# Kernel optimization log

Measured on AMD Instinct MI355X. Metric: run time of the kernel, lower is better.

## Reference

```python
import jax, jax.numpy as jnp
import numpy as np

N_STATE = 64
SEQ_L = 4096
BATCH, HCH = 16, 512
DT_MIN, DT_MAX = 0.001, 0.1


def _make_DPLR_HiPPO(N):
    # HiPPO-LegS matrix and its NPLR -> DPLR decomposition (annotated-s4).
    P = np.sqrt(1 + 2 * np.arange(N))
    A = P[:, None] * P[None, :]
    A = np.tril(A) - np.diag(np.arange(N))
    nhippo = -A
    p = 0.5 * np.sqrt(2 * np.arange(1, N + 1) + 1.0)
    q = 2 * p
    S = nhippo + p[:, None] * q[None, :]
    Lambda, V = np.linalg.eig(S)
    Vc = V.conj().T
    p_t = Vc @ p
    q_t = Vc @ q.conj()
    return Lambda, p_t, q_t, Vc


def _ri(z):
    return np.stack([z.real, z.imag], axis=-1).astype(np.float32)


def setup_inputs() -> dict:
    key = jax.random.key(0)
    k_u, k_ct, k_b, k_d, k_ls = jax.random.split(key, 5)
    Lambda, p, q, Vc = _make_DPLR_HiPPO(N_STATE)
    u = jax.random.normal(k_u, (BATCH, HCH, SEQ_L), dtype=jnp.float32)
    # lecun_normal params (fan_in = N)
    Ct_ri = jax.random.normal(k_ct, (1, N_STATE, 2), dtype=jnp.float32) / np.sqrt(N_STATE)
    Bp = jax.random.normal(k_b, (N_STATE, 1), dtype=jnp.float32) / np.sqrt(N_STATE)
    D = jax.random.uniform(k_d, (1,), dtype=jnp.float32)
    log_step = jax.random.uniform(
        k_ls, (1,), dtype=jnp.float32,
        minval=np.log(DT_MIN), maxval=np.log(DT_MAX))
    return {
        "u": u,
        "Lambda_ri": jnp.asarray(_ri(Lambda)),
        "p_ri": jnp.asarray(_ri(p)),
        "q_ri": jnp.asarray(_ri(q)),
        "Vc_ri": jnp.asarray(_ri(Vc)),
        "Ct_ri": Ct_ri,
        "Bp": Bp,
        "D": D,
        "log_step": log_step,
    }


def _cplx(x_ri):
    return x_ri[..., 0] + 1j * x_ri[..., 1]


def _s4_kernel(Lambda, p, q, B, Ct, step, L):
    # DPLR generating function evaluated at the L roots of unity (K_gen_DPLR
    # + conv_from_gen), vectorized over frequencies.
    Omega = jnp.exp((-2j * jnp.pi) * (jnp.arange(L) / L))          # (L,)
    g = (2.0 / step) * ((1.0 - Omega) / (1.0 + Omega))             # (L,)
    c = 2.0 / (1.0 + Omega)                                        # (L,)
    denom = g[:, None] - Lambda[None, :]                           # (L, N)
    cauchy = lambda v: (v[None, :] / denom).sum(-1)                # (L,)
    k00 = cauchy(Ct.conj() * B)
    k01 = cauchy(Ct.conj() * p)
    k10 = cauchy(q.conj() * B)
    k11 = cauchy(q.conj() * p)
    at_roots = c * (k00 - k01 * (1.0 / (1.0 + k11)) * k10)
    return jnp.fft.ifft(at_roots, L).real                          # (L,)


def reference(u, Lambda_ri, p_ri, q_ri, Vc_ri, Ct_ri, Bp, D, log_step):
    L = u.shape[-1]
    Lambda = _cplx(Lambda_ri)
    p = _cplx(p_ri)
    q = _cplx(q_ri)
    Vc = _cplx(Vc_ri)
    Ct = _cplx(Ct_ri).reshape(-1)                  # (N,)
    B = (Vc @ Bp.astype(Vc.dtype)).reshape(-1)     # (N,) complex
    step = jnp.exp(log_step)[0]
    K = _s4_kernel(Lambda, p, q, B, Ct, step, L).astype(u.dtype)   # (L,)
    # non-circular convolution via zero-padded FFT along the last axis
    n = 2 * L
    y = jnp.fft.irfft(jnp.fft.rfft(u, n=n) * jnp.fft.rfft(K, n=n), n=n)[..., :L]
    return y + D[0] * u
```

## Files before the change

### kernel.cpp

```cpp
#include <hip/hip_runtime.h>
#include <math.h>


#define SEQ_L 4096
#define M4    4096
#define NFFT  8192
#define NST   64
#define NROWS 8192
#define TWO_PI 6.28318530717958647692f

typedef float2 cf;

__device__ __forceinline__ cf cmul(cf a, cf b){ return make_float2(a.x*b.x - a.y*b.y, a.x*b.y + a.y*b.x); }
__device__ __forceinline__ cf cadd(cf a, cf b){ return make_float2(a.x+b.x, a.y+b.y); }
__device__ __forceinline__ cf csub(cf a, cf b){ return make_float2(a.x-b.x, a.y-b.y); }
__device__ __forceinline__ double2 dcmul(double2 a, double2 b) {
  return make_double2(a.x*b.x - a.y*b.y, a.x*b.y + a.y*b.x);
}

__device__ __forceinline__ int s2f(int i){ return i ^ (((i >> 6) & 1) << 3); }
__device__ __forceinline__ int s3f(int i){ return i ^ ((i >> 6) & 7) ^ (((i >> 6) & 1) << 3); }
__device__ __forceinline__ int smf(int i){ return i ^ ((i >> 6) & 7); }
__device__ __forceinline__ int sw(int p){ return p ^ ((p >> 4) & 15); }

template<int S>
__device__ __forceinline__ void r4(cf& a0, cf& a1, cf& a2, cf& a3){
  cf t0 = cadd(a0,a2), t1 = csub(a0,a2);
  cf t2 = cadd(a1,a3), t3 = csub(a1,a3);
  cf w = (S < 0) ? make_float2(t3.y, -t3.x) : make_float2(-t3.y, t3.x);
  a0 = cadd(t0,t2); a2 = csub(t0,t2);
  a1 = cadd(t1,w);  a3 = csub(t1,w);
}

template<int S, bool ZHI, bool LO4=false>
__device__ __forceinline__ void dft8(cf x[8]){
  const float C = 0.70710678118654752f;
  cf e0,e1,e2,e3,o0,o1,o2,o3;
  if (ZHI) {
    cf w  = (S<0)? make_float2(x[2].y,-x[2].x) : make_float2(-x[2].y,x[2].x);
    e0 = cadd(x[0],x[2]); e2 = csub(x[0],x[2]);
    e1 = cadd(x[0],w);    e3 = csub(x[0],w);
    cf w2 = (S<0)? make_float2(x[3].y,-x[3].x) : make_float2(-x[3].y,x[3].x);
    o0 = cadd(x[1],x[3]); o2 = csub(x[1],x[3]);
    o1 = cadd(x[1],w2);   o3 = csub(x[1],w2);
  } else {
    cf a0=x[0],a1=x[2],a2=x[4],a3=x[6];
    r4<S>(a0,a1,a2,a3);  e0=a0;e1=a1;e2=a2;e3=a3;
    cf b0=x[1],b1=x[3],b2=x[5],b3=x[7];
    r4<S>(b0,b1,b2,b3);  o0=b0;o1=b1;o2=b2;o3=b3;
  }
  x[0] = cadd(e0,o0); if (!LO4) x[4] = csub(e0,o0);
  cf t1 = (S<0)? make_float2(C*(o1.x+o1.y), C*(o1.y-o1.x))
               : make_float2(C*(o1.x-o1.y), C*(o1.x+o1.y));
  x[1] = cadd(e1,t1); if (!LO4) x[5] = csub(e1,t1);
  cf t2 = (S<0)? make_float2(o2.y,-o2.x) : make_float2(-o2.y,o2.x);
  x[2] = cadd(e2,t2); if (!LO4) x[6] = csub(e2,t2);
  cf t3 = (S<0)? make_float2(C*(o3.y-o3.x), -C*(o3.x+o3.y))
               : make_float2(-C*(o3.x+o3.y), C*(o3.x-o3.y));
  x[3] = cadd(e3,t3); if (!LO4) x[7] = csub(e3,t3);
}

__device__ __forceinline__ void chain8(cf x[8], float th){
  float sn, cs; __sincosf(th, &sn, &cs);
  cf w1 = make_float2(cs, sn);
  cf w2 = cmul(w1, w1);
  cf w3 = cmul(w2, w1);
  x[1] = cmul(x[1], w1); x[2] = cmul(x[2], w2); x[3] = cmul(x[3], w3);
  cf w4 = cmul(w2, w2);
  cf w5 = cmul(w3, w2);
  cf w6 = cmul(w3, w3);
  cf w7 = cmul(w4, w3);
  x[4] = cmul(x[4], w4); x[5] = cmul(x[5], w5); x[6] = cmul(x[6], w6);
  x[7] = cmul(x[7], w7);
}

__device__ __forceinline__ constexpr float c16t(int d){
  return (d==1)?0.92387953251128675613f:(d==2)?0.70710678118654752440f:
         (d==3)?0.38268343236508977173f:(d==4)?0.f:
         (d==5)?-0.38268343236508977173f:(d==6)?-0.70710678118654752440f:
         -0.92387953251128675613f;
}
__device__ __forceinline__ constexpr float s16t(int d){
  return (d==1)?0.38268343236508977173f:(d==2)?0.70710678118654752440f:
         (d==3)?0.92387953251128675613f:(d==4)?1.f:
         (d==5)?0.92387953251128675613f:(d==6)?0.70710678118654752440f:
         0.38268343236508977173f;
}
template<int S>
__device__ __forceinline__ void tw16(cf x[8], int t000){
  #pragma unroll
  for (int d = 1; d < 8; ++d) {
    float ce = t000 ? c16t(d) : 1.f;
    float se = t000 ? ((S < 0) ? -s16t(d) : s16t(d)) : 0.f;
    cf a = x[d];
    x[d] = make_float2(a.x*ce - a.y*se, a.x*se + a.y*ce);
  }
}

__device__ __forceinline__ void r2_shfl(cf x[8], int tid){
  const float sgn = (tid & 1) ? -1.f : 1.f;
  #pragma unroll
  for (int k = 0; k < 8; ++k) {
    float ox = __shfl_xor(x[k].x, 1, 64);
    float oy = __shfl_xor(x[k].y, 1, 64);
    x[k].x = ox + sgn * x[k].x;
    x[k].y = oy + sgn * x[k].y;
  }
}

__global__ __launch_bounds__(256) void k_at(
    const float* __restrict__ Lam_ri, const float* __restrict__ p_ri,
    const float* __restrict__ q_ri,  const float* __restrict__ Vc_ri,
    const float* __restrict__ Ct_ri, const float* __restrict__ Bp,
    const float* __restrict__ log_step, float2* __restrict__ atroots) {
  __shared__ double2 lam[NST], ctB[NST], ctp[NST], qB[NST], qp[NST];
  __shared__ double stepd;
  int tx = threadIdx.x;
  if (tx < NST) {
    int n = tx;
    double lr = Lam_ri[2*n], li = Lam_ri[2*n+1];
    double pr = p_ri[2*n],  pi = p_ri[2*n+1];
    double qr = q_ri[2*n],  qi = q_ri[2*n+1];
    double cr = Ct_ri[2*n], ci = Ct_ri[2*n+1];
    double br = 0.0, bi = 0.0;
    for (int m = 0; m < NST; ++m) {
      double b = (double)Bp[m];
      br += (double)Vc_ri[2*(n*NST+m)]   * b;
      bi += (double)Vc_ri[2*(n*NST+m)+1] * b;
    }
    lam[n] = make_double2(lr, li);
    ctB[n] = make_double2(cr*br + ci*bi, cr*bi - ci*br);
    ctp[n] = make_double2(cr*pr + ci*pi, cr*pi - ci*pr);
    qB[n]  = make_double2(qr*br + qi*bi, qr*bi - qi*br);
    qp[n]  = make_double2(qr*pr + qi*pi, qr*pi - qi*pr);
  }
  if (tx == 0) stepd = exp((double)log_step[0]);
  __syncthreads();
  int l = blockIdx.x * 256 + tx;
  double ang = -2.0 * M_PI * (double)l / (double)SEQ_L;
  double sn, cs;
  sincos(ang, &sn, &cs);
  double2 onem = make_double2(1.0 - cs, -sn);
  double2 onep = make_double2(1.0 + cs,  sn);
  double den = onep.x*onep.x + onep.y*onep.y;
  double2 ip = make_double2(onep.x/den, -onep.y/den);
  double2 g  = dcmul(onem, ip);
  double tw = 2.0 / stepd;
  g.x *= tw; g.y *= tw;
  double2 cc = make_double2(2.0*ip.x, 2.0*ip.y);
  double2 k00 = make_double2(0,0), k01 = make_double2(0,0);
  double2 k10 = make_double2(0,0), k11 = make_double2(0,0);
  for (int n = 0; n < NST; ++n) {
    double2 L = lam[n];
    double2 d = make_double2(g.x - L.x, g.y - L.y);
    double dd = d.x*d.x + d.y*d.y;
    double2 inv = make_double2(d.x/dd, -d.y/dd);
    double2 v;
    v = ctB[n]; k00.x += v.x*inv.x - v.y*inv.y; k00.y += v.x*inv.y + v.y*inv.x;
    v = ctp[n]; k01.x += v.x*inv.x - v.y*inv.y; k01.y += v.x*inv.y + v.y*inv.x;
    v = qB[n];  k10.x += v.x*inv.x - v.y*inv.y; k10.y += v.x*inv.y + v.y*inv.x;
    v = qp[n];  k11.x += v.x*inv.x - v.y*inv.y; k11.y += v.x*inv.y + v.y*inv.x;
  }
  double2 k11p = make_double2(1.0 + k11.x, k11.y);
  double2 num  = dcmul(k01, k10);
  double dd2 = k11p.x*k11p.x + k11p.y*k11p.y;
  double2 t = make_double2((num.x*k11p.x + num.y*k11p.y)/dd2,
                           (num.y*k11p.x - num.x*k11p.y)/dd2);
  double2 inner = make_double2(k00.x - t.x, k00.y - t.y);
  double2 at = dcmul(cc, inner);
  atroots[l] = make_float2((float)at.x, (float)at.y);
}

__global__ __launch_bounds__(512) void k_kt(const float2* __restrict__ atroots,
                                            float* __restrict__ Kt) {
  int gid  = blockIdx.x * 512 + threadIdx.x;
  int t    = gid >> 6;
  int lane = gid & 63;
  float acc = 0.f;
  for (int l = lane; l < SEQ_L; l += 64) {
    int ph = (l * t) & (SEQ_L - 1);
    float a = (float)ph * (TWO_PI / (float)SEQ_L);
    float sn, cs; __sincosf(a, &sn, &cs);
    float2 v = atroots[l];
    acc += v.x*cs - v.y*sn;
  }
  for (int off = 32; off > 0; off >>= 1) acc += __shfl_down(acc, off, 64);
  if (lane == 0) Kt[t] = acc * (1.0f / (float)SEQ_L);
}

__global__ __launch_bounds__(1024) void k_G(const float* __restrict__ Kt,
                                            float2* __restrict__ G) {
  __shared__ cf lds[NFFT];
  int tid = threadIdx.x;
  cf x[8];
  #pragma unroll
  for (int m = 0; m < 4; ++m) x[m] = make_float2(Kt[tid + 1024*m], 0.f);
  #pragma unroll
  for (int m = 4; m < 8; ++m) x[m] = make_float2(0.f, 0.f);
  const int a1 = tid >> 7, t0 = tid & 127, b2 = (tid >> 4) & 7, t00 = tid & 15;
  const int c3 = (tid >> 1) & 7, t000 = tid & 1;
  dft8<-1, true>(x);
  chain8(x, -TWO_PI * (float)tid / (float)NFFT);
  #pragma unroll
  for (int a = 0; a < 8; ++a) lds[sw(a*1024 + tid)] = x[a];
  __syncthreads();
  #pragma unroll
  for (int r = 0; r < 8; ++r) x[r] = lds[sw(a1*1024 + t0 + 128*r)];
  dft8<-1, false>(x);
  chain8(x, -TWO_PI * (float)t0 / 1024.f);
  __syncthreads();
  #pragma unroll
  for (int b = 0; b < 8; ++b) lds[sw(a1*1024 + b*128 + t0)] = x[b];
  __syncthreads();
  #pragma unroll
  for (int r = 0; r < 8; ++r) x[r] = lds[sw(a1*1024 + b2*128 + t00 + 16*r)];
  dft8<-1, false>(x);
  chain8(x, -TWO_PI * (float)t00 / 128.f);
  __syncthreads();
  #pragma unroll
  for (int c = 0; c < 8; ++c) lds[sw(a1*1024 + b2*128 + c*16 + t00)] = x[c];
  __syncthreads();
  #pragma unroll
  for (int r = 0; r < 8; ++r) x[r] = lds[sw(a1*1024 + b2*128 + c3*16 + t000 + 2*r)];
  dft8<-1, false>(x);
  tw16<-1>(x, t000);
  r2_shfl(x, tid);
  #pragma unroll
  for (int d = 0; d < 8; ++d) {
    int bin = a1 + 8*b2 + 64*c3 + 512*d + 4096*t000;
    if (bin <= M4) G[bin] = x[d];
  }
}

__global__ __launch_bounds__(256) void k_ab(const float2* __restrict__ G,
                                            float4* __restrict__ ab) {
  int idx = blockIdx.x * 256 + threadIdx.x;
  int tidc = idx >> 3, d = idx & 7;
  int k = (tidc >> 6) + 8*((tidc >> 3) & 7) + 64*(tidc & 7) + 512*d;
  double ang = -2.0 * M_PI * (double)k / (double)NFFT;
  double sn, cs; sincos(ang, &sn, &cs);
  double2 a = make_double2(0.5*(1.0 + sn), -0.5*cs);
  double2 b = make_double2(0.5*(1.0 - sn),  0.5*cs);
  double2 p = make_double2(0.5*(1.0 + sn),  0.5*cs);
  double2 q = make_double2(0.5*(1.0 - sn), -0.5*cs);
  float2 gk = G[k];
  float2 gh = G[M4 - k];
  double2 Gk = make_double2(gk.x, gk.y);
  double2 Gh = make_double2(gh.x, -gh.y);
  double2 pa = dcmul(p, a), pb = dcmul(p, b);
  double2 qa = dcmul(q, a), qb = dcmul(q, b);
  double2 al = dcmul(pa, Gk), t1 = dcmul(qb, Gh);
  al.x += t1.x; al.y += t1.y;
  double2 be = dcmul(pb, Gk), t2 = dcmul(qa, Gh);
  be.x += t2.x; be.y += t2.y;
  const double s = 1.0 / (double)M4;
  ab[idx] = make_float4((float)(al.x*s), (float)(al.y*s),
                        (float)(be.x*s), (float)(be.y*s));
}

__global__ __launch_bounds__(512) void k_conv(const float* __restrict__ u,
                                              const float4* __restrict__ ab,
                                              const float* __restrict__ Dp,
                                              float* __restrict__ out) {
  __shared__ cf lds[M4];
  const int tid = threadIdx.x;
  const size_t row = blockIdx.x;
  const float2* ru = (const float2*)(u + row * SEQ_L);
  const int a1 = tid >> 6, t0 = tid & 63, b2 = (tid >> 3) & 7, t00 = tid & 7;

  cf x[8];
  #pragma unroll
  for (int m = 0; m < 4; ++m) { float2 v = ru[tid + 512*m]; x[m] = make_float2(v.x, v.y); }
  #pragma unroll
  for (int m = 4; m < 8; ++m) x[m] = make_float2(0.f, 0.f);

  dft8<-1, true>(x);
  chain8(x, -TWO_PI * (float)tid / (float)M4);
  #pragma unroll
  for (int a = 0; a < 8; ++a) lds[a*512 + tid] = x[a];
  __syncthreads();
  #pragma unroll
  for (int r = 0; r < 8; ++r) x[r] = lds[a1*512 + t0 + 64*r];
  dft8<-1, false>(x);
  chain8(x, -TWO_PI * (float)t0 / 512.f);
  __syncthreads();
  #pragma unroll
  for (int b = 0; b < 8; ++b) lds[s2f(a1*512 + b*64 + t0)] = x[b];
  __syncthreads();
  #pragma unroll
  for (int r = 0; r < 8; ++r) x[r] = lds[s2f(a1*512 + b2*64 + t00 + 8*r)];
  dft8<-1, false>(x);
  chain8(x, -TWO_PI * (float)t00 / 64.f);
  __syncthreads();
  #pragma unroll
  for (int c = 0; c < 8; ++c) lds[s3f(a1*512 + b2*64 + c*8 + t00)] = x[c];
  __syncthreads();
  #pragma unroll
  for (int r = 0; r < 8; ++r) x[r] = lds[s3f(a1*512 + b2*64 + t00*8 + r)];
  dft8<-1, false>(x);
  __syncthreads();

  const int base = a1 + 8*b2 + 64*t00;
  #pragma unroll
  for (int d = 0; d < 8; ++d) lds[smf(base + 512*d)] = x[d];
  __syncthreads();
  const float4* abp = ab + (size_t)tid * 8;
  #pragma unroll
  for (int d = 0; d < 8; ++d) {
    cf t = lds[smf((M4 - base - 512*d) & (M4 - 1))];
    float4 c = abp[d];
    x[d] = make_float2(c.x*x[d].x - c.y*x[d].y + c.z*t.x + c.w*t.y,
                       c.x*x[d].y + c.y*x[d].x + c.w*t.x - c.z*t.y);
  }
  __syncthreads();

  dft8<1, false>(x);
  #pragma unroll
  for (int r = 0; r < 8; ++r) lds[s3f(a1*512 + b2*64 + t00*8 + r)] = x[r];
  __syncthreads();
  #pragma unroll
  for (int c = 0; c < 8; ++c) x[c] = lds[s3f(a1*512 + b2*64 + c*8 + t00)];
  chain8(x, TWO_PI * (float)t00 / 64.f);
  dft8<1, false>(x);
  __syncthreads();
  #pragma unroll
  for (int r = 0; r < 8; ++r) lds[s2f(a1*512 + b2*64 + t00 + 8*r)] = x[r];
  __syncthreads();
  #pragma unroll
  for (int b = 0; b < 8; ++b) x[b] = lds[s2f(a1*512 + b*64 + t0)];
  chain8(x, TWO_PI * (float)t0 / 512.f);
  dft8<1, false>(x);
  __syncthreads();
  #pragma unroll
  for (int r = 0; r < 8; ++r) lds[a1*512 + t0 + 64*r] = x[r];
  __syncthreads();
  #pragma unroll
  for (int a = 0; a < 8; ++a) x[a] = lds[a*512 + tid];
  chain8(x, TWO_PI * (float)tid / (float)M4);
  dft8<1, false, true>(x);

  const float Dv = Dp[0];
  float2* o = (float2*)(out + row * SEQ_L);
  #pragma unroll
  for (int m = 0; m < 4; ++m) {
    float2 uv = ru[tid + 512*m];
    o[tid + 512*m] = make_float2(x[m].x + Dv*uv.x, x[m].y + Dv*uv.y);
  }
}

extern "C" void kernel_launch(void* const* d_in, const int* in_sizes, int n_in,
                              void* d_out, int out_size, void* d_ws, size_t ws_size,
                              hipStream_t stream) {
  const float* u      = (const float*)d_in[0];
  const float* Lam_ri = (const float*)d_in[1];
  const float* p_ri   = (const float*)d_in[2];
  const float* q_ri   = (const float*)d_in[3];
  const float* Vc_ri  = (const float*)d_in[4];
  const float* Ct_ri  = (const float*)d_in[5];
  const float* Bp     = (const float*)d_in[6];
  const float* Dp     = (const float*)d_in[7];
  const float* ls     = (const float*)d_in[8];

  char* ws = (char*)d_ws;
  float2* atroots = (float2*)(ws);
  float*  Kt      = (float*) (ws + 32768);
  float2* G       = (float2*)(ws + 49152);
  float4* ab      = (float4*)(ws + 81936);

  k_at  <<<dim3(SEQ_L/256), dim3(256), 0, stream>>>(Lam_ri, p_ri, q_ri, Vc_ri, Ct_ri, Bp, ls, atroots);
  k_kt  <<<dim3(512),  dim3(512), 0, stream>>>(atroots, Kt);
  k_G   <<<dim3(1),    dim3(1024), 0, stream>>>(Kt, G);
  k_ab  <<<dim3(16),   dim3(256), 0, stream>>>(G, ab);
  k_conv<<<dim3(NROWS), dim3(512), 0, stream>>>(u, ab, Dp, (float*)d_out);
}
```

Measured before the change: 198.6 us.

## Replace direct inverse DFT with in-block FFT and fuse kernel-prep stages

The O(L^2) sincos-based inverse DFT in k_kt is replaced by a radix-8 4096-point inverse FFT inside a single 1024-thread block. That block also performs the 8192-point forward FFT and the real-FFT split coefficients (former k_G and k_ab), passing intermediates through LDS instead of global memory. This removes two kernel launches and the quadratic DFT work. The cost is that the inverse FFT runs on only one workgroup, with half its threads idle during that phase, so the serial prep latency on one CU grows.

New measurement: 184.3 us (median of 2 runs). 7.2% less time.

```diff
diff --git a/kernel.cpp b/kernel.cpp
--- a/kernel.cpp
+++ b/kernel.cpp
@@ -171,91 +171,126 @@
   atroots[l] = make_float2((float)at.x, (float)at.y);
 }
 
-__global__ __launch_bounds__(512) void k_kt(const float2* __restrict__ atroots,
-                                            float* __restrict__ Kt) {
-  int gid  = blockIdx.x * 512 + threadIdx.x;
-  int t    = gid >> 6;
-  int lane = gid & 63;
-  float acc = 0.f;
-  for (int l = lane; l < SEQ_L; l += 64) {
-    int ph = (l * t) & (SEQ_L - 1);
-    float a = (float)ph * (TWO_PI / (float)SEQ_L);
-    float sn, cs; __sincosf(a, &sn, &cs);
-    float2 v = atroots[l];
-    acc += v.x*cs - v.y*sn;
-  }
-  for (int off = 32; off > 0; off >>= 1) acc += __shfl_down(acc, off, 64);
-  if (lane == 0) Kt[t] = acc * (1.0f / (float)SEQ_L);
-}
-
-__global__ __launch_bounds__(1024) void k_G(const float* __restrict__ Kt,
-                                            float2* __restrict__ G) {
-  __shared__ cf lds[NFFT];
-  int tid = threadIdx.x;
+__global__ __launch_bounds__(1024) void k_Gab(const float2* __restrict__ at,
+                                              float4* __restrict__ ab) {
+  __shared__ cf lds8[NFFT];
+  float* ktf = (float*)(lds8 + 4096);
+  const int tid = threadIdx.x;
+  const bool act = tid < 512;
+  const int a14 = tid >> 6, t04 = tid & 63, b24 = (tid >> 3) & 7, t004 = tid & 7;
   cf x[8];
-  #pragma unroll
-  for (int m = 0; m < 4; ++m) x[m] = make_float2(Kt[tid + 1024*m], 0.f);
-  #pragma unroll
-  for (int m = 4; m < 8; ++m) x[m] = make_float2(0.f, 0.f);
-  const int a1 = tid >> 7, t0 = tid & 127, b2 = (tid >> 4) & 7, t00 = tid & 15;
-  const int c3 = (tid >> 1) & 7, t000 = tid & 1;
-  dft8<-1, true>(x);
-  chain8(x, -TWO_PI * (float)tid / (float)NFFT);
-  #pragma unroll
-  for (int a = 0; a < 8; ++a) lds[sw(a*1024 + tid)] = x[a];
-  __syncthreads();
-  #pragma unroll
-  for (int r = 0; r < 8; ++r) x[r] = lds[sw(a1*1024 + t0 + 128*r)];
-  dft8<-1, false>(x);
-  chain8(x, -TWO_PI * (float)t0 / 1024.f);
-  __syncthreads();
-  #pragma unroll
-  for (int b = 0; b < 8; ++b) lds[sw(a1*1024 + b*128 + t0)] = x[b];
-  __syncthreads();
-  #pragma unroll
-  for (int r = 0; r < 8; ++r) x[r] = lds[sw(a1*1024 + b2*128 + t00 + 16*r)];
-  dft8<-1, false>(x);
-  chain8(x, -TWO_PI * (float)t00 / 128.f);
-  __syncthreads();
-  #pragma unroll
-  for (int c = 0; c < 8; ++c) lds[sw(a1*1024 + b2*128 + c*16 + t00)] = x[c];
-  __syncthreads();
-  #pragma unroll
-  for (int r = 0; r < 8; ++r) x[r] = lds[sw(a1*1024 + b2*128 + c3*16 + t000 + 2*r)];
-  dft8<-1, false>(x);
-  tw16<-1>(x, t000);
-  r2_shfl(x, tid);
-  #pragma unroll
-  for (int d = 0; d < 8; ++d) {
-    int bin = a1 + 8*b2 + 64*c3 + 512*d + 4096*t000;
-    if (bin <= M4) G[bin] = x[d];
-  }
-}
-
-__global__ __launch_bounds__(256) void k_ab(const float2* __restrict__ G,
-                                            float4* __restrict__ ab) {
-  int idx = blockIdx.x * 256 + threadIdx.x;
-  int tidc = idx >> 3, d = idx & 7;
-  int k = (tidc >> 6) + 8*((tidc >> 3) & 7) + 64*(tidc & 7) + 512*d;
-  double ang = -2.0 * M_PI * (double)k / (double)NFFT;
-  double sn, cs; sincos(ang, &sn, &cs);
-  double2 a = make_double2(0.5*(1.0 + sn), -0.5*cs);
-  double2 b = make_double2(0.5*(1.0 - sn),  0.5*cs);
-  double2 p = make_double2(0.5*(1.0 + sn),  0.5*cs);
-  double2 q = make_double2(0.5*(1.0 - sn), -0.5*cs);
-  float2 gk = G[k];
-  float2 gh = G[M4 - k];
-  double2 Gk = make_double2(gk.x, gk.y);
-  double2 Gh = make_double2(gh.x, -gh.y);
-  double2 pa = dcmul(p, a), pb = dcmul(p, b);
-  double2 qa = dcmul(q, a), qb = dcmul(q, b);
-  double2 al = dcmul(pa, Gk), t1 = dcmul(qb, Gh);
-  al.x += t1.x; al.y += t1.y;
-  double2 be = dcmul(pb, Gk), t2 = dcmul(qa, Gh);
-  be.x += t2.x; be.y += t2.y;
-  const double s = 1.0 / (double)M4;
-  ab[idx] = make_float4((float)(al.x*s), (float)(al.y*s),
-                        (float)(be.x*s), (float)(be.y*s));
+
+  if (act) {
+    #pragma unroll
+    for (int m = 0; m < 8; ++m) x[m] = at[tid + 512*m];
+    dft8<1, false>(x);
+    chain8(x, TWO_PI * (float)tid / (float)M4);
+    #pragma unroll
+    for (int a = 0; a < 8; ++a) lds8[a*512 + tid] = x[a];
+  }
+  __syncthreads();
+  if (act) {
+    #pragma unroll
+    for (int r = 0; r < 8; ++r) x[r] = lds8[a14*512 + t04 + 64*r];
+    dft8<1, false>(x);
+    chain8(x, TWO_PI * (float)t04 / 512.f);
+  }
+  __syncthreads();
+  if (act) {
+    #pragma unroll
+    for (int b = 0; b < 8; ++b) lds8[s2f(a14*512 + b*64 + t04)] = x[b];
+  }
+  __syncthreads();
+  if (act) {
+    #pragma unroll
+    for (int r = 0; r < 8; ++r) x[r] = lds8[s2f(a14*512 + b24*64 + t004 + 8*r)];
+    dft8<1, false>(x);
+    chain8(x, TWO_PI * (float)t004 / 64.f);
+  }
+  __syncthreads();
+  if (act) {
+    #pragma unroll
+    for (int c = 0; c < 8; ++c) lds8[s3f(a14*512 + b24*64 + c*8 + t004)] = x[c];
+  }
+  __syncthreads();
+  if (act) {
+    #pragma unroll
+    for (int r = 0; r < 8; ++r) x[r] = lds8[s3f(a14*512 + b24*64 + t004*8 + r)];
+    dft8<1, false>(x);
+    const int tb = a14 + 8*b24 + 64*t004;
+    #pragma unroll
+    for (int d = 0; d < 8; ++d) ktf[tb + 512*d] = x[d].x * (1.f/(float)M4);
+  }
+  __syncthreads();
+
+  {
+    const int a1 = tid >> 7, t0 = tid & 127, b2 = (tid >> 4) & 7, t00 = tid & 15;
+    const int c3 = (tid >> 1) & 7, t000 = tid & 1;
+    #pragma unroll
+    for (int m = 0; m < 4; ++m) x[m] = make_float2(ktf[tid + 1024*m], 0.f);
+    #pragma unroll
+    for (int m = 4; m < 8; ++m) x[m] = make_float2(0.f, 0.f);
+    dft8<-1, true>(x);
+    chain8(x, -TWO_PI * (float)tid / (float)NFFT);
+    __syncthreads();
+    #pragma unroll
+    for (int a = 0; a < 8; ++a) lds8[sw(a*1024 + tid)] = x[a];
+    __syncthreads();
+    #pragma unroll
+    for (int r = 0; r < 8; ++r) x[r] = lds8[sw(a1*1024 + t0 + 128*r)];
+    dft8<-1, false>(x);
+    chain8(x, -TWO_PI * (float)t0 / 1024.f);
+    __syncthreads();
+    #pragma unroll
+    for (int b = 0; b < 8; ++b) lds8[sw(a1*1024 + b*128 + t0)] = x[b];
+    __syncthreads();
+    #pragma unroll
+    for (int r = 0; r < 8; ++r) x[r] = lds8[sw(a1*1024 + b2*128 + t00 + 16*r)];
+    dft8<-1, false>(x);
+    chain8(x, -TWO_PI * (float)t00 / 128.f);
+    __syncthreads();
+    #pragma unroll
+    for (int c = 0; c < 8; ++c) lds8[sw(a1*1024 + b2*128 + c*16 + t00)] = x[c];
+    __syncthreads();
+    #pragma unroll
+    for (int r = 0; r < 8; ++r) x[r] = lds8[sw(a1*1024 + b2*128 + c3*16 + t000 + 2*r)];
+    dft8<-1, false>(x);
+    tw16<-1>(x, t000);
+    r2_shfl(x, tid);
+    __syncthreads();
+    #pragma unroll
+    for (int d = 0; d < 8; ++d) {
+      int bin = a1 + 8*b2 + 64*c3 + 512*d + 4096*t000;
+      if (bin <= M4) lds8[bin] = x[d];
+    }
+  }
+  __syncthreads();
+
+  #pragma unroll
+  for (int j = 0; j < 4; ++j) {
+    int idx = tid * 4 + j;
+    int tidc = idx >> 3, d = idx & 7;
+    int k = (tidc >> 6) + 8*((tidc >> 3) & 7) + 64*(tidc & 7) + 512*d;
+    double ang = -2.0 * M_PI * (double)k / (double)NFFT;
+    double sn, cs; sincos(ang, &sn, &cs);
+    double2 a = make_double2(0.5*(1.0 + sn), -0.5*cs);
+    double2 b = make_double2(0.5*(1.0 - sn),  0.5*cs);
+    double2 p = make_double2(0.5*(1.0 + sn),  0.5*cs);
+    double2 q = make_double2(0.5*(1.0 - sn), -0.5*cs);
+    cf gk = lds8[k];
+    cf gh = lds8[M4 - k];
+    double2 Gk = make_double2(gk.x, gk.y);
+    double2 Gh = make_double2(gh.x, -gh.y);
+    double2 pa = dcmul(p, a), pb = dcmul(p, b);
+    double2 qa = dcmul(q, a), qb = dcmul(q, b);
+    double2 al = dcmul(pa, Gk), t1 = dcmul(qb, Gh);
+    al.x += t1.x; al.y += t1.y;
+    double2 be = dcmul(pb, Gk), t2 = dcmul(qa, Gh);
+    be.x += t2.x; be.y += t2.y;
+    const double s = 1.0 / (double)M4;
+    ab[idx] = make_float4((float)(al.x*s), (float)(al.y*s),
+                          (float)(be.x*s), (float)(be.y*s));
+  }
 }
 
 __global__ __launch_bounds__(512) void k_conv(const float* __restrict__ u,
@@ -363,13 +398,9 @@
 
   char* ws = (char*)d_ws;
   float2* atroots = (float2*)(ws);
-  float*  Kt      = (float*) (ws + 32768);
-  float2* G       = (float2*)(ws + 49152);
-  float4* ab      = (float4*)(ws + 81936);
+  float4* ab      = (float4*)(ws + 32768);
 
   k_at  <<<dim3(SEQ_L/256), dim3(256), 0, stream>>>(Lam_ri, p_ri, q_ri, Vc_ri, Ct_ri, Bp, ls, atroots);
-  k_kt  <<<dim3(512),  dim3(512), 0, stream>>>(atroots, Kt);
-  k_G   <<<dim3(1),    dim3(1024), 0, stream>>>(Kt, G);
-  k_ab  <<<dim3(16),   dim3(256), 0, stream>>>(G, ab);
+  k_Gab <<<dim3(1),    dim3(1024), 0, stream>>>(atroots, ab);
   k_conv<<<dim3(NROWS), dim3(512), 0, stream>>>(u, ab, Dp, (float*)d_out);
 }
```
